# Kernel optimization log

Measured on AMD Instinct MI355X. Metric: run time of the kernel, lower is better.

## Reference

```python
import jax, jax.numpy as jnp
import numpy as np

TOP_K = 2  # num_experts_per_tok


def setup_inputs() -> dict:
    key = jax.random.key(0)
    ks = jax.random.split(key, 5)
    B, T, D, H, E = 32, 1024, 512, 2048, 8
    scale_in = 1.0 / np.sqrt(D)
    scale_h = 1.0 / np.sqrt(H)
    return {
        "x": jax.random.normal(ks[0], (B, T, D), dtype=jnp.float32),
        "gate_w": jax.random.normal(ks[1], (D, E), dtype=jnp.float32) * scale_in,
        "gate_b": jnp.zeros((E,), dtype=jnp.float32),
        "w1": jax.random.normal(ks[2], (E, D, H), dtype=jnp.float32) * scale_in,
        "b1": jnp.zeros((E, H), dtype=jnp.float32),
        "w2": jax.random.normal(ks[3], (E, H, D), dtype=jnp.float32) * scale_h,
        "b2": jnp.zeros((E, D), dtype=jnp.float32),
    }


def reference(x, gate_w, gate_b, w1, b1, w2, b2):
    # Per-sample routing: pool over time, gate -> [B, E]
    pooled = x.mean(axis=1)                                   # [B, D]
    gate_logits = pooled @ gate_w + gate_b                    # [B, E]
    topk_w, topk_idx = jax.lax.top_k(gate_logits, TOP_K)      # [B, K]
    topk_w = jax.nn.softmax(topk_w.astype(jnp.float32), axis=1).astype(x.dtype)

    out = jnp.zeros_like(x)
    for k in range(TOP_K):  # small fixed loop over top-k slots
        idx = topk_idx[:, k]                                  # [B] expert id per sample
        # gather expert weights per sample (irregular access)
        h = jax.nn.silu(jnp.einsum('btd,bdh->bth', x, w1[idx]) + b1[idx][:, None, :])
        y = jnp.einsum('bth,bhd->btd', h, w2[idx]) + b2[idx][:, None, :]
        out = out + topk_w[:, k, None, None] * y
    out = out + x  # use_residual=True
    return out, gate_logits
```

## Files before the change

kernel.cpp:

```cpp
#include <hip/hip_runtime.h>
#include <stdint.h>

typedef unsigned short u16;
typedef __attribute__((ext_vector_type(8))) short short8;
typedef __attribute__((ext_vector_type(8))) u16 ushort8;
typedef __attribute__((ext_vector_type(4))) float f32x4;

#define B_ 32
#define T_ 1024
#define D_ 512
#define H_ 2048
#define E_ 8

__device__ __forceinline__ u16 f2bf(float f) {
  union { float f; uint32_t u; } v; v.f = f;
  uint32_t u = v.u;
  uint32_t r = (u + 0x7fffu + ((u >> 16) & 1u)) >> 16;
  return (u16)r;
}

__device__ __forceinline__ void gload16(const void* g, void* l) {
  __builtin_amdgcn_global_load_lds(
      (const __attribute__((address_space(1))) unsigned int*)g,
      (__attribute__((address_space(3))) unsigned int*)l, 16, 0, 0);
}


__global__ void k_convert_x(const float* __restrict__ in, u16* __restrict__ out, int n8) {
  int i = blockIdx.x * 256 + threadIdx.x;
  if (i >= n8) return;
  const float4* p = reinterpret_cast<const float4*>(in) + (size_t)i * 2;
  float4 a = p[0], b = p[1];
  ushort8 r;
  r[0] = f2bf(a.x); r[1] = f2bf(a.y); r[2] = f2bf(a.z); r[3] = f2bf(a.w);
  r[4] = f2bf(b.x); r[5] = f2bf(b.y); r[6] = f2bf(b.z); r[7] = f2bf(b.w);
  reinterpret_cast<ushort8*>(out)[i] = r;
}

__global__ void k_transpose_bf16(const float* __restrict__ in, u16* __restrict__ out,
                                 int R, int C) {
  __shared__ float tile[64][65];
  int e = blockIdx.z;
  int c0 = blockIdx.x * 64, r0 = blockIdx.y * 64;
  const float* src = in + (size_t)e * R * C;
  u16* dst = out + (size_t)e * R * C;
  int t = threadIdx.x;
#pragma unroll
  for (int i = 0; i < 16; i++) {
    int idx = i * 256 + t;
    int r = idx >> 6, c = idx & 63;
    tile[r][c] = src[(size_t)(r0 + r) * C + (c0 + c)];
  }
  __syncthreads();
#pragma unroll
  for (int i = 0; i < 16; i++) {
    int idx = i * 256 + t;
    int c = idx >> 6, r = idx & 63;
    dst[(size_t)(c0 + c) * R + (r0 + r)] = f2bf(tile[r][c]);
  }
}


__global__ void k_pool_partial(const float* __restrict__ x, float* __restrict__ partial) {
  int b = blockIdx.y, c = blockIdx.x, t = threadIdx.x;
  const float* xp = x + ((size_t)b * T_ + c * 16) * D_;
  float s0 = 0.f, s1 = 0.f;
#pragma unroll
  for (int r = 0; r < 16; r++) {
    s0 += xp[r * D_ + t];
    s1 += xp[r * D_ + t + 256];
  }
  partial[((size_t)b * 64 + c) * D_ + t] = s0;
  partial[((size_t)b * 64 + c) * D_ + t + 256] = s1;
}

__global__ void k_gate(const float* __restrict__ partial, const float* __restrict__ gate_w,
                       const float* __restrict__ gate_b, float* __restrict__ gate_out,
                       int* __restrict__ eidx, float* __restrict__ ewt) {
  int b = blockIdx.x, t = threadIdx.x;
  __shared__ float pooled[D_];
  __shared__ float logits[E_];
  for (int d = t; d < D_; d += 256) {
    float s = 0.f;
    for (int c = 0; c < 64; c++) s += partial[((size_t)b * 64 + c) * D_ + d];
    pooled[d] = s * (1.0f / 1024.0f);
  }
  __syncthreads();
  if (t < E_) {
    float s = gate_b[t];
    for (int d = 0; d < D_; d++) s += pooled[d] * gate_w[d * E_ + t];
    logits[t] = s;
    gate_out[b * E_ + t] = s;
  }
  __syncthreads();
  if (t == 0) {
    int i1 = 0; float v1 = logits[0];
    for (int e = 1; e < E_; e++) if (logits[e] > v1) { v1 = logits[e]; i1 = e; }
    int i2 = -1; float v2 = -3.4e38f;
    for (int e = 0; e < E_; e++) {
      if (e == i1) continue;
      if (logits[e] > v2) { v2 = logits[e]; i2 = e; }
    }
    float e1 = __expf(v2 - v1);
    float den = 1.0f / (1.0f + e1);
    eidx[b * 2 + 0] = i1; eidx[b * 2 + 1] = i2;
    ewt[b * 2 + 0] = den; ewt[b * 2 + 1] = e1 * den;
  }
}

template <int N, int K, int MODE>
__global__ __launch_bounds__(512, 2)
void moe_gemm8(const u16* __restrict__ A, const u16* __restrict__ W,
               const float* __restrict__ bias, u16* __restrict__ Hout,
               float* __restrict__ Out, const float* __restrict__ Xres,
               const int* __restrict__ eidx, const float* __restrict__ ewt,
               int kpick, int bofs) {
  extern __shared__ u16 lds[];
  constexpr int NT = K / 32;
  constexpr int NTN = N / 256;
  const int ib = blockIdx.y;
  const int b = ib + bofs;
  const int tm = blockIdx.x / NTN, tn = blockIdx.x % NTN;
  const int e = eidx[b * 2 + kpick];
  const int tid = threadIdx.x;
  const int wave = tid >> 6, ln = tid & 63, hi = ln >> 4, l15 = ln & 15;
  const int wr = wave >> 2, wc = wave & 3;

  u16* As = lds;
  u16* Bs = lds + 32768;

  const u16* Ab = A + (size_t)ib * T_ * K + (size_t)(tm * 256) * K;
  const u16* Wb = W + (size_t)e * N * K + (size_t)(tn * 256) * K;

  const int row0 = tid >> 2;
  const int row1 = 128 + row0;
  const int ch0 = (tid & 3) ^ ((row0 >> 1) & 3);
  const int ch1 = (tid & 3) ^ ((row1 >> 1) & 3);
  const int ldsw0 = wave * 512;
  const int ldsw1 = 4096 + wave * 512;

  auto stageA = [&](int t) {
    const u16* g = Ab + t * 32;
    u16* l = As + (t & 3) * 8192;
    gload16(g + (size_t)row0 * K + ch0 * 8, l + ldsw0);
    gload16(g + (size_t)row1 * K + ch1 * 8, l + ldsw1);
  };
  auto stageB = [&](int t) {
    const u16* g = Wb + t * 32;
    u16* l = Bs + (t & 3) * 8192;
    gload16(g + (size_t)row0 * K + ch0 * 8, l + ldsw0);
    gload16(g + (size_t)row1 * K + ch1 * 8, l + ldsw1);
  };
  auto readA = [&](int bi, int m) -> short8 {
    const int r = wr * 128 + m * 16 + l15;
    const int cp = hi ^ ((r >> 1) & 3);
    return *reinterpret_cast<const short8*>(As + bi * 8192 + r * 32 + cp * 8);
  };
  auto readB = [&](int bi, int n) -> short8 {
    const int r = wc * 64 + n * 16 + l15;
    const int cp = hi ^ ((r >> 1) & 3);
    return *reinterpret_cast<const short8*>(Bs + bi * 8192 + r * 32 + cp * 8);
  };

  f32x4 acc[8][4] = {};

  stageA(0); stageB(0);
  stageA(1); stageB(1);
  stageA(2); stageB(2);
  asm volatile("s_waitcnt vmcnt(8)" ::: "memory");
  __builtin_amdgcn_s_barrier();
  __builtin_amdgcn_sched_barrier(0);

  for (int tb = 0; tb < NT; tb += 4) {
#pragma unroll
    for (int u = 0; u < 4; u++) {
      const int t = tb + u;
      const int bi = u;
      short8 af[4], bfr[4];
#pragma unroll
      for (int m = 0; m < 4; m++) af[m] = readA(bi, m);
#pragma unroll
      for (int n = 0; n < 4; n++) bfr[n] = readB(bi, n);
      if (t + 3 < NT) stageA(t + 3);
      __builtin_amdgcn_s_barrier();
      __builtin_amdgcn_sched_barrier(0);
      __builtin_amdgcn_s_setprio(1);
#pragma unroll
      for (int m = 0; m < 4; m++)
#pragma unroll
        for (int n = 0; n < 4; n++)
          acc[m][n] = __builtin_amdgcn_mfma_f32_16x16x32_bf16(af[m], bfr[n], acc[m][n], 0, 0, 0);
      __builtin_amdgcn_s_setprio(0);
      __builtin_amdgcn_s_barrier();
#pragma unroll
      for (int m = 0; m < 4; m++) af[m] = readA(bi, m + 4);
      if (t + 3 < NT) stageB(t + 3);
      __builtin_amdgcn_s_barrier();
      __builtin_amdgcn_sched_barrier(0);
      __builtin_amdgcn_s_setprio(1);
#pragma unroll
      for (int m = 0; m < 4; m++)
#pragma unroll
        for (int n = 0; n < 4; n++)
          acc[m + 4][n] = __builtin_amdgcn_mfma_f32_16x16x32_bf16(af[m], bfr[n], acc[m + 4][n], 0, 0, 0);
      __builtin_amdgcn_s_setprio(0);
      if (t < NT - 3)      { asm volatile("s_waitcnt vmcnt(8)" ::: "memory"); }
      else if (t == NT - 3){ asm volatile("s_waitcnt vmcnt(4)" ::: "memory"); }
      else if (t == NT - 2){ asm volatile("s_waitcnt vmcnt(0)" ::: "memory"); }
      __builtin_amdgcn_s_barrier();
      __builtin_amdgcn_sched_barrier(0);
    }
  }

  const float* be = bias + (size_t)e * N;
  if (MODE == 0) {
    u16* Hb = Hout + (size_t)ib * T_ * N;
#pragma unroll
    for (int m = 0; m < 8; m++) {
#pragma unroll
      for (int n = 0; n < 4; n++) {
        const int col = tn * 256 + wc * 64 + n * 16 + l15;
        const float bv = be[col];
#pragma unroll
        for (int j = 0; j < 4; j++) {
          const int row = tm * 256 + wr * 128 + m * 16 + hi * 4 + j;
          float z = acc[m][n][j] + bv;
          float hv = z / (1.0f + expf(-z));
          Hb[(size_t)row * N + col] = f2bf(hv);
        }
      }
    }
  } else {
    const float wt = ewt[b * 2 + kpick];
    float* Ob = Out + (size_t)b * T_ * D_;
    const float* Xb = Xres + (size_t)b * T_ * D_;
#pragma unroll
    for (int m = 0; m < 8; m++) {
#pragma unroll
      for (int n = 0; n < 4; n++) {
        const int col = tn * 256 + wc * 64 + n * 16 + l15;
        const float bv = be[col];
#pragma unroll
        for (int j = 0; j < 4; j++) {
          const int row = tm * 256 + wr * 128 + m * 16 + hi * 4 + j;
          float y = acc[m][n][j] + bv;
          size_t o = (size_t)row * D_ + col;
          float base = (kpick == 0) ? Xb[o] : Ob[o];
          Ob[o] = base + wt * y;
        }
      }
    }
  }
}


extern "C" void kernel_launch(void* const* d_in, const int* in_sizes, int n_in,
                              void* d_out, int out_size, void* d_ws, size_t ws_size,
                              hipStream_t stream) {
  (void)in_sizes; (void)n_in; (void)out_size;
  const float* x      = (const float*)d_in[0];
  const float* gate_w = (const float*)d_in[1];
  const float* gate_b = (const float*)d_in[2];
  const float* w1     = (const float*)d_in[3];
  const float* b1     = (const float*)d_in[4];
  const float* w2     = (const float*)d_in[5];
  const float* b2     = (const float*)d_in[6];
  float* out = (float*)d_out;
  float* gate_out = out + (size_t)B_ * T_ * D_;

  char* ws = (char*)d_ws;
  size_t off = 0;
  auto alloc = [&](size_t bytes) -> void* {
    void* p = ws + off;
    off += (bytes + 255) & ~(size_t)255;
    return p;
  };
  u16* x16     = (u16*)alloc((size_t)B_ * T_ * D_ * 2);
  u16* w1t     = (u16*)alloc((size_t)E_ * H_ * D_ * 2);
  u16* w2t     = (u16*)alloc((size_t)E_ * D_ * H_ * 2);
  float* part  = (float*)alloc((size_t)B_ * 64 * D_ * 4);
  int* eidx    = (int*)alloc(B_ * 2 * sizeof(int));
  float* ewt   = (float*)alloc(B_ * 2 * sizeof(float));
  int BCH = 32;
  while (BCH > 1 && off + (size_t)BCH * T_ * H_ * 2 > ws_size) BCH >>= 1;
  u16* h = (u16*)alloc((size_t)BCH * T_ * H_ * 2);

  constexpr int LDSB = 131072;
  (void)hipFuncSetAttribute((const void*)moe_gemm8<H_, D_, 0>,
                            hipFuncAttributeMaxDynamicSharedMemorySize, LDSB);
  (void)hipFuncSetAttribute((const void*)moe_gemm8<D_, H_, 1>,
                            hipFuncAttributeMaxDynamicSharedMemorySize, LDSB);

  k_convert_x<<<dim3((B_ * T_ * D_ / 8) / 256), 256, 0, stream>>>(x, x16, B_ * T_ * D_ / 8);
  k_transpose_bf16<<<dim3(H_ / 64, D_ / 64, E_), 256, 0, stream>>>(w1, w1t, D_, H_);
  k_transpose_bf16<<<dim3(D_ / 64, H_ / 64, E_), 256, 0, stream>>>(w2, w2t, H_, D_);
  k_pool_partial<<<dim3(64, B_), 256, 0, stream>>>(x, part);
  k_gate<<<B_, 256, 0, stream>>>(part, gate_w, gate_b, gate_out, eidx, ewt);

  for (int bofs = 0; bofs < B_; bofs += BCH) {
    for (int k = 0; k < 2; k++) {
      moe_gemm8<H_, D_, 0><<<dim3((T_ / 256) * (H_ / 256), BCH), 512, LDSB, stream>>>(
          x16 + (size_t)bofs * T_ * D_, w1t, b1, h, nullptr, nullptr, eidx, ewt, k, bofs);
      moe_gemm8<D_, H_, 1><<<dim3((T_ / 256) * (D_ / 256), BCH), 512, LDSB, stream>>>(
          h, w2t, b2, nullptr, out, x, eidx, ewt, k, bofs);
    }
  }
}
```

Baseline: 715.4 us.

## Software-pipeline LDS fragment reads, cut barriers, vectorize transposed epilogue

Restructures the GEMM main loop so the next tile's LDS fragments are read into double-buffered registers while the current tile's MFMAs run, with one barrier per tile instead of three. Global staging of A and B for tile t+3 is issued together. The MFMA operand order is swapped so each lane holds four consecutive output columns, which lets the epilogue use vector bias loads, 4-wide bf16 stores, vector float4 residual read-modify-write, and a fast rcp/exp SiLU. This adds register pressure and depends on the vmcnt accounting staying correct.

Result: faster. 605.3 us (-15.4%).

```diff
diff --git a/kernel.cpp b/kernel.cpp
--- a/kernel.cpp
+++ b/kernel.cpp
@@ -4,6 +4,7 @@
 typedef unsigned short u16;
 typedef __attribute__((ext_vector_type(8))) short short8;
 typedef __attribute__((ext_vector_type(8))) u16 ushort8;
+typedef __attribute__((ext_vector_type(4))) u16 u16x4;
 typedef __attribute__((ext_vector_type(4))) float f32x4;
 
 #define B_ 32
@@ -107,6 +108,31 @@
     ewt[b * 2 + 0] = den; ewt[b * 2 + 1] = e1 * den;
   }
 }
+
+
+#define TILE_BODY(BFC, BFN, T, DOSTAGE, DORD, VMODE) do {                      \
+  const int sc_ = ((T) & 3) * 8192, sn_ = (((T) + 1) & 3) * 8192;              \
+  _Pragma("unroll") for (int m_ = 0; m_ < 4; m_++) a4[m_] = rdA(sc_, m_ + 4);  \
+  if (DORD) { _Pragma("unroll") for (int n_ = 0; n_ < 4; n_++) BFN[n_] = rdB(sn_, n_); } \
+  if (DOSTAGE) { stageA((T) + 3); stageB((T) + 3); }                           \
+  __builtin_amdgcn_sched_barrier(0);                                           \
+  __builtin_amdgcn_s_setprio(1);                                               \
+  _Pragma("unroll") for (int m_ = 0; m_ < 4; m_++)                             \
+    _Pragma("unroll") for (int n_ = 0; n_ < 4; n_++)                           \
+      acc[m_][n_] = __builtin_amdgcn_mfma_f32_16x16x32_bf16(BFC[n_], a0[m_], acc[m_][n_], 0, 0, 0); \
+  __builtin_amdgcn_s_setprio(0);                                               \
+  if (DORD) { _Pragma("unroll") for (int m_ = 0; m_ < 4; m_++) a0[m_] = rdA(sn_, m_); } \
+  __builtin_amdgcn_sched_barrier(0);                                           \
+  __builtin_amdgcn_s_setprio(1);                                               \
+  _Pragma("unroll") for (int m_ = 0; m_ < 4; m_++)                             \
+    _Pragma("unroll") for (int n_ = 0; n_ < 4; n_++)                           \
+      acc[m_ + 4][n_] = __builtin_amdgcn_mfma_f32_16x16x32_bf16(BFC[n_], a4[m_], acc[m_ + 4][n_], 0, 0, 0); \
+  __builtin_amdgcn_s_setprio(0);                                               \
+  if ((VMODE) == 1) { asm volatile("s_waitcnt vmcnt(4)" ::: "memory"); }       \
+  else if ((VMODE) == 0) { asm volatile("s_waitcnt vmcnt(0)" ::: "memory"); }  \
+  __builtin_amdgcn_s_barrier();                                                \
+  __builtin_amdgcn_sched_barrier(0);                                           \
+} while (0)
 
 template <int N, int K, int MODE>
 __global__ __launch_bounds__(512, 2)
@@ -151,103 +177,77 @@
     gload16(g + (size_t)row0 * K + ch0 * 8, l + ldsw0);
     gload16(g + (size_t)row1 * K + ch1 * 8, l + ldsw1);
   };
-  auto readA = [&](int bi, int m) -> short8 {
+  auto rdA = [&](int so, int m) -> short8 {
     const int r = wr * 128 + m * 16 + l15;
     const int cp = hi ^ ((r >> 1) & 3);
-    return *reinterpret_cast<const short8*>(As + bi * 8192 + r * 32 + cp * 8);
-  };
-  auto readB = [&](int bi, int n) -> short8 {
+    return *reinterpret_cast<const short8*>(As + so + r * 32 + cp * 8);
+  };
+  auto rdB = [&](int so, int n) -> short8 {
     const int r = wc * 64 + n * 16 + l15;
     const int cp = hi ^ ((r >> 1) & 3);
-    return *reinterpret_cast<const short8*>(Bs + bi * 8192 + r * 32 + cp * 8);
+    return *reinterpret_cast<const short8*>(Bs + so + r * 32 + cp * 8);
   };
 
   f32x4 acc[8][4] = {};
+  short8 a0[4], a4[4], bfA[4], bfB[4];
 
   stageA(0); stageB(0);
   stageA(1); stageB(1);
   stageA(2); stageB(2);
-  asm volatile("s_waitcnt vmcnt(8)" ::: "memory");
+  asm volatile("s_waitcnt vmcnt(4)" ::: "memory");
   __builtin_amdgcn_s_barrier();
   __builtin_amdgcn_sched_barrier(0);
-
-  for (int tb = 0; tb < NT; tb += 4) {
-#pragma unroll
-    for (int u = 0; u < 4; u++) {
-      const int t = tb + u;
-      const int bi = u;
-      short8 af[4], bfr[4];
-#pragma unroll
-      for (int m = 0; m < 4; m++) af[m] = readA(bi, m);
-#pragma unroll
-      for (int n = 0; n < 4; n++) bfr[n] = readB(bi, n);
-      if (t + 3 < NT) stageA(t + 3);
-      __builtin_amdgcn_s_barrier();
-      __builtin_amdgcn_sched_barrier(0);
-      __builtin_amdgcn_s_setprio(1);
-#pragma unroll
-      for (int m = 0; m < 4; m++)
-#pragma unroll
-        for (int n = 0; n < 4; n++)
-          acc[m][n] = __builtin_amdgcn_mfma_f32_16x16x32_bf16(af[m], bfr[n], acc[m][n], 0, 0, 0);
-      __builtin_amdgcn_s_setprio(0);
-      __builtin_amdgcn_s_barrier();
-#pragma unroll
-      for (int m = 0; m < 4; m++) af[m] = readA(bi, m + 4);
-      if (t + 3 < NT) stageB(t + 3);
-      __builtin_amdgcn_s_barrier();
-      __builtin_amdgcn_sched_barrier(0);
-      __builtin_amdgcn_s_setprio(1);
-#pragma unroll
-      for (int m = 0; m < 4; m++)
-#pragma unroll
-        for (int n = 0; n < 4; n++)
-          acc[m + 4][n] = __builtin_amdgcn_mfma_f32_16x16x32_bf16(af[m], bfr[n], acc[m + 4][n], 0, 0, 0);
-      __builtin_amdgcn_s_setprio(0);
-      if (t < NT - 3)      { asm volatile("s_waitcnt vmcnt(8)" ::: "memory"); }
-      else if (t == NT - 3){ asm volatile("s_waitcnt vmcnt(4)" ::: "memory"); }
-      else if (t == NT - 2){ asm volatile("s_waitcnt vmcnt(0)" ::: "memory"); }
-      __builtin_amdgcn_s_barrier();
-      __builtin_amdgcn_sched_barrier(0);
-    }
-  }
-
-  const float* be = bias + (size_t)e * N;
+#pragma unroll
+  for (int m = 0; m < 4; m++) a0[m] = rdA(0, m);
+#pragma unroll
+  for (int n = 0; n < 4; n++) bfA[n] = rdB(0, n);
+
+  for (int t = 0; t < NT - 4; t += 2) {
+    TILE_BODY(bfA, bfB, t,     true,  true,  1);
+    TILE_BODY(bfB, bfA, t + 1, true,  true,  1);
+  }
+  TILE_BODY(bfA, bfB, NT - 4, true,  true,  1);
+  TILE_BODY(bfB, bfA, NT - 3, false, true,  0);
+  TILE_BODY(bfA, bfB, NT - 2, false, true,  -1);
+  TILE_BODY(bfB, bfA, NT - 1, false, false, -1);
+
+  const float* be = bias + (size_t)e * N + tn * 256 + wc * 64 + hi * 4;
+  f32x4 bv[4];
+#pragma unroll
+  for (int n = 0; n < 4; n++) bv[n] = *reinterpret_cast<const f32x4*>(be + n * 16);
+
   if (MODE == 0) {
-    u16* Hb = Hout + (size_t)ib * T_ * N;
+    u16* Hb = Hout + (size_t)ib * T_ * N +
+              (size_t)(tm * 256 + wr * 128 + l15) * N + tn * 256 + wc * 64 + hi * 4;
 #pragma unroll
     for (int m = 0; m < 8; m++) {
+      u16* Hr = Hb + (size_t)m * 16 * N;
 #pragma unroll
       for (int n = 0; n < 4; n++) {
-        const int col = tn * 256 + wc * 64 + n * 16 + l15;
-        const float bv = be[col];
+        u16x4 o;
 #pragma unroll
         for (int j = 0; j < 4; j++) {
-          const int row = tm * 256 + wr * 128 + m * 16 + hi * 4 + j;
-          float z = acc[m][n][j] + bv;
-          float hv = z / (1.0f + expf(-z));
-          Hb[(size_t)row * N + col] = f2bf(hv);
+          float z = acc[m][n][j] + bv[n][j];
+          float hv = z * __builtin_amdgcn_rcpf(1.0f + __expf(-z));
+          o[j] = f2bf(hv);
         }
+        *reinterpret_cast<u16x4*>(Hr + n * 16) = o;
       }
     }
   } else {
     const float wt = ewt[b * 2 + kpick];
-    float* Ob = Out + (size_t)b * T_ * D_;
-    const float* Xb = Xres + (size_t)b * T_ * D_;
+    const size_t rowoff = (size_t)(tm * 256 + wr * 128 + l15) * D_ + tn * 256 + wc * 64 + hi * 4;
+    float* Ob = Out + (size_t)b * T_ * D_ + rowoff;
+    const float* Xb = Xres + (size_t)b * T_ * D_ + rowoff;
 #pragma unroll
     for (int m = 0; m < 8; m++) {
 #pragma unroll
       for (int n = 0; n < 4; n++) {
-        const int col = tn * 256 + wc * 64 + n * 16 + l15;
-        const float bv = be[col];
-#pragma unroll
-        for (int j = 0; j < 4; j++) {
-          const int row = tm * 256 + wr * 128 + m * 16 + hi * 4 + j;
-          float y = acc[m][n][j] + bv;
-          size_t o = (size_t)row * D_ + col;
-          float base = (kpick == 0) ? Xb[o] : Ob[o];
-          Ob[o] = base + wt * y;
-        }
+        const size_t o = (size_t)m * 16 * D_ + n * 16;
+        f32x4 y = acc[m][n] + bv[n];
+        f32x4 base = (kpick == 0) ? *reinterpret_cast<const f32x4*>(Xb + o)
+                                  : *reinterpret_cast<const f32x4*>(Ob + o);
+        *reinterpret_cast<f32x4*>(Ob + o) = base + wt * y;
       }
     }
   }
```
